# Kernel tuning notes

Hardware: AMD Instinct MI355X
Metric: run time of the kernel (lower is better)

Reference implementation:

```python
import jax, jax.numpy as jnp
import numpy as np

B, N, DIM = 2, 8192, 3
K = 16            # num_neighbours (dilation=1)
R = 2048          # num_representitives
CIN, CL, COUT = 64, 16, 128
K2 = K * K


def _bn(x, g, b):
    # BatchNorm in eval mode with running_mean=0, running_var=1 -> affine
    return x * g + b


def setup_inputs() -> dict:
    key = jax.random.key(0)
    ks = jax.random.split(key, 24)
    r = lambda i, shape, s=1.0: jax.random.normal(ks[i], shape, jnp.float32) * s
    return {
        "points": r(0, (B, N, DIM)),
        "features": r(1, (B, N, CIN)),
        "lift_w": r(2, (CL, DIM), 0.3), "lift_b": r(3, (CL,), 0.1),
        "bn_lift_g": 1.0 + r(4, (CL,), 0.1), "bn_lift_b": r(5, (CL,), 0.1),
        "t1_w": r(6, (K2, DIM * K), 0.1), "t1_b": r(7, (K2,), 0.1),
        "bn1_g": 1.0 + r(8, (K2,), 0.1), "bn1_b": r(9, (K2,), 0.1),
        "t2_w": r(10, (K2, K2), 0.05), "t2_b": r(11, (K2,), 0.1),
        "bn2_g": 1.0 + r(12, (K2,), 0.1), "bn2_b": r(13, (K2,), 0.1),
        "t3_w": r(14, (K2, K2), 0.05), "t3_b": r(15, (K2,), 0.1),
        "bn3_g": 1.0 + r(16, (K2,), 0.1), "bn3_b": r(17, (K2,), 0.1),
        "conv_w": r(18, (COUT, CIN + CL, K), 0.05), "conv_b": r(19, (COUT,), 0.1),
        "rep_idx": jax.random.permutation(ks[20], N)[:R],
    }


def reference(points, features, lift_w, lift_b, bn_lift_g, bn_lift_b,
              t1_w, t1_b, bn1_g, bn1_b, t2_w, t2_b, bn2_g, bn2_b,
              t3_w, t3_b, bn3_g, bn3_b, conv_w, conv_b, rep_idx):
    b, n, _ = points.shape
    # ---- KNN (squared distance is order-equivalent to torch.cdist) ----
    sq = jnp.sum(points * points, -1)                                   # (b,n)
    d2 = sq[:, :, None] + sq[:, None, :] - 2.0 * jnp.einsum('bnd,bmd->bnm', points, points)
    _, idx = jax.lax.top_k(-d2, K + 1)                                  # (b,n,K+1)
    nn_idx = idx[:, :, 1:]                                              # drop self
    # ---- representative sampling + neighbor gather ----
    rep_pos = points[:, rep_idx]                                        # (b,R,3)
    nb_idx = nn_idx[:, rep_idx]                                         # (b,R,K)
    gather = jax.vmap(lambda arr, i: arr[i])
    nbr_pos = gather(points, nb_idx)                                    # (b,R,K,3)
    nbr_feat = gather(features, nb_idx)                                 # (b,R,K,CIN)
    # ---- X_conv ----
    p = (nbr_pos - rep_pos[:, :, None, :]).reshape(b * R, K, DIM)       # centered
    lifted = jax.nn.relu(_bn(p @ lift_w.T + lift_b, bn_lift_g, bn_lift_b))  # (bR,K,CL)
    feat = jnp.concatenate([lifted, nbr_feat.reshape(b * R, K, CIN)], -1)   # (bR,K,CL+CIN)
    pf = p.reshape(b * R, K * DIM)
    h = jax.nn.relu(_bn(pf @ t1_w.T + t1_b, bn1_g, bn1_b))
    h = jax.nn.relu(_bn(h @ t2_w.T + t2_b, bn2_g, bn2_b))
    T = _bn(h @ t3_w.T + t3_b, bn3_g, bn3_b).reshape(b * R, K, K)       # learned transform
    Tf = jnp.einsum('bij,bjc->bic', T, feat)                            # bmm, (bR,K,C)
    # Conv1d(C, COUT, kernel=K) over length K -> single output position
    out = jnp.einsum('bkc,ock->bo', Tf, conv_w) + conv_b                # (bR,COUT)
    return rep_pos, out.reshape(b, R, COUT)
```

## Files before the change

### kernel.cpp

```cpp
#include <hip/hip_runtime.h>
#include <float.h>

#define Bn 2
#define Nn 8192
#define Rr 2048
#define Kk 16
#define CIN 64
#define CL 16
#define COUT 128
#define K2c 256
#define GT (Bn*Rr)
#define FD (CL+CIN)
#define KC (Kk*FD)
#define MG 8

__global__ __launch_bounds__(256) void prep_kernel(
    const float* __restrict__ t1_w, const float* __restrict__ t2_w,
    const float* __restrict__ t3_w, const float* __restrict__ conv_w,
    const float* __restrict__ points,
    float* __restrict__ t1t, float* __restrict__ t2t,
    float* __restrict__ t3t, float* __restrict__ wp,
    float4* __restrict__ pts4)
{
  int i = blockIdx.x * 256 + threadIdx.x;
  if (i < K2c*48) { int j = i / 48, k = i - j*48; t1t[k*K2c + j] = t1_w[i]; }
  if (i < K2c*K2c) { int j = i >> 8, k = i & 255; t2t[k*K2c + j] = t2_w[i]; t3t[k*K2c + j] = t3_w[i]; }
  if (i < COUT*KC) {
    int o = i / KC, ck = i - o*KC;
    int c = ck >> 4, k = ck & 15;
    wp[(k*FD + c)*COUT + o] = conv_w[i];
  }
  if (i < Bn*Nn) {
    float x = points[i*3+0], y = points[i*3+1], z = points[i*3+2];
    float sq = __fadd_rn(__fadd_rn(__fmul_rn(x,x), __fmul_rn(y,y)), __fmul_rn(z,z));
    pts4[i] = make_float4(x, y, z, sq);
  }
}

__global__ __launch_bounds__(512) void knn_kernel(
    const float4* __restrict__ pts4, const int* __restrict__ rep_idx,
    int* __restrict__ nb_idx, float* __restrict__ p_out,
    float* __restrict__ rep_pos_out)
{
  __shared__ float4 ptsS[3072];
  __shared__ unsigned long long coll[8][128];
  int t    = threadIdx.x;
  int lane = t & 63;
  int w    = t >> 6;
  int g    = blockIdx.x * 8 + w;
  int b    = g >> 11;
  int r    = g & 2047;
  int n    = rep_idx[r];
  const float4* pb4 = pts4 + (size_t)b*Nn;
  float4 Q = pb4[n];
  float qx = Q.x, qy = Q.y, qz = Q.z, sqn = Q.w;

  float c0 = FLT_MAX, c1 = FLT_MAX, c2 = FLT_MAX;
  for (int c = 0; c < 3; c++) {
    int base  = c * 3072;
    int count = (c < 2) ? 3072 : 2048;
    __syncthreads();
    for (int i = t; i < count; i += 512) ptsS[i] = pb4[base + i];
    __syncthreads();
    int iters = count >> 6;
    #pragma unroll 4
    for (int j = 0; j < iters; j++) {
      float4 P = ptsS[j*64 + lane];
      float dot = __fmaf_rn(qz, P.z, __fmaf_rn(qy, P.y, __fmul_rn(qx, P.x)));
      float d2  = __fsub_rn(__fadd_rn(sqn, P.w), __fmul_rn(2.0f, dot));
      float nc2 = __builtin_amdgcn_fmed3f(c1, c2, d2);
      float nc1 = __builtin_amdgcn_fmed3f(c0, c1, d2);
      float nc0 = fminf(c0, d2);
      c0 = nc0; c1 = nc1; c2 = nc2;
    }
  }

  float tau = FLT_MAX;
  for (int rnd = 0; rnd < 17; rnd++) {
    float m = c0;
    #pragma unroll
    for (int off = 1; off < 64; off <<= 1) m = fminf(m, __shfl_xor(m, off));
    if (c0 == m) { c0 = c1; c1 = c2; c2 = FLT_MAX; }
    tau = m;
  }

  int cnt = 0;
  for (int c = 0; c < 3; c++) {
    int base  = c * 3072;
    int count = (c < 2) ? 3072 : 2048;
    __syncthreads();
    for (int i = t; i < count; i += 512) ptsS[i] = pb4[base + i];
    __syncthreads();
    int iters = count >> 6;
    #pragma unroll 4
    for (int j = 0; j < iters; j++) {
      float4 P = ptsS[j*64 + lane];
      float dot = __fmaf_rn(qz, P.z, __fmaf_rn(qy, P.y, __fmul_rn(qx, P.x)));
      float d2  = __fsub_rn(__fadd_rn(sqn, P.w), __fmul_rn(2.0f, dot));
      bool pr = (d2 <= tau);
      unsigned long long mask = __ballot(pr);
      if (pr) {
        int pos = cnt + (int)__popcll(mask & ((1ull << lane) - 1ull));
        if (pos < 128) {
          unsigned f = __float_as_uint(d2);
          unsigned mono = f ^ ((unsigned)((int)f >> 31) | 0x80000000u);
          coll[w][pos] = ((unsigned long long)mono << 32) | (unsigned)(base + j*64 + lane);
        }
      }
      cnt += (int)__popcll(mask);
    }
  }
  if (cnt > 128) cnt = 128;

  unsigned long long e1 = (lane < cnt)      ? coll[w][lane]      : ~0ull;
  unsigned long long e2 = (lane + 64 < cnt) ? coll[w][lane + 64] : ~0ull;
  int out_m = 0;
  for (int rnd = 0; rnd < 17; rnd++) {
    unsigned long long myk = (e1 < e2) ? e1 : e2;
    unsigned long long kmin = myk;
    #pragma unroll
    for (int off = 1; off < 64; off <<= 1) {
      unsigned long long o = __shfl_xor(kmin, off);
      kmin = (o < kmin) ? o : kmin;
    }
    if (rnd >= 1 && lane == rnd - 1) out_m = (int)(kmin & 0xFFFFFFFFull);
    if (kmin == e1) e1 = ~0ull;
    else if (kmin == e2) e2 = ~0ull;
  }

  if (lane < 16) {
    nb_idx[g*Kk + lane] = out_m;
    float4 P = pb4[out_m];
    p_out[(g*Kk + lane)*3 + 0] = __fsub_rn(P.x, qx);
    p_out[(g*Kk + lane)*3 + 1] = __fsub_rn(P.y, qy);
    p_out[(g*Kk + lane)*3 + 2] = __fsub_rn(P.z, qz);
  }
  if (lane < 3) rep_pos_out[g*3 + lane] = (lane == 0 ? qx : (lane == 1 ? qy : qz));
}

__device__ __forceinline__ void fma_g(float4& a, float hv, const float4& wv) {
  a.x = fmaf(hv, wv.x, a.x);
  a.y = fmaf(hv, wv.y, a.y);
  a.z = fmaf(hv, wv.z, a.z);
  a.w = fmaf(hv, wv.w, a.w);
}

__global__ __launch_bounds__(256) void mlp_kernel(
    const float* __restrict__ p,
    const float* __restrict__ t1t, const float* __restrict__ t1_b,
    const float* __restrict__ g1v, const float* __restrict__ b1v,
    const float* __restrict__ t2t, const float* __restrict__ t2_b,
    const float* __restrict__ g2v, const float* __restrict__ b2v,
    const float* __restrict__ t3t, const float* __restrict__ t3_b,
    const float* __restrict__ g3v, const float* __restrict__ b3v,
    float* __restrict__ T_out)
{
  __shared__ float pf[48][MG];
  __shared__ float hA[K2c][MG];
  __shared__ float red[4][64][36];
  int t = threadIdx.x;
  int w = t >> 6, l = t & 63;
  int g0 = blockIdx.x * MG;
  for (int e = t; e < MG*48; e += 256) {
    int g = e / 48, k = e - g*48;
    pf[k][g] = p[(size_t)(g0+g)*48 + k];
  }
  __syncthreads();

  float4 acc[8];

#define KLOOP(WSRC, KDIM, HBUF)                                        \
  {                                                                    \
    _Pragma("unroll")                                                  \
    for (int q = 0; q < 8; q++) acc[q] = make_float4(0.f,0.f,0.f,0.f); \
    float4 wb0 = *(const float4*)&WSRC[(size_t)w*K2c + 4*l];           \
    float4 wb1 = (w + 4 < KDIM) ?                                      \
        *(const float4*)&WSRC[(size_t)(w+4)*K2c + 4*l] : wb0;          \
    _Pragma("unroll 2")                                                \
    for (int k = w; k < KDIM; k += 4) {                                \
      float4 wc = wb0; wb0 = wb1;                                      \
      if (k + 8 < KDIM)                                                \
        wb1 = *(const float4*)&WSRC[(size_t)(k+8)*K2c + 4*l];          \
      float4 h0 = *(const float4*)&HBUF[k][0];                         \
      float4 h1 = *(const float4*)&HBUF[k][4];                         \
      fma_g(acc[0], h0.x, wc); fma_g(acc[1], h0.y, wc);                \
      fma_g(acc[2], h0.z, wc); fma_g(acc[3], h0.w, wc);                \
      fma_g(acc[4], h1.x, wc); fma_g(acc[5], h1.y, wc);                \
      fma_g(acc[6], h1.z, wc); fma_g(acc[7], h1.w, wc);                \
    }                                                                  \
  }

#define WRITE_RED()                                                        \
  {                                                                        \
    float4 ra, rb;                                                         \
    ra = make_float4(acc[0].x, acc[1].x, acc[2].x, acc[3].x);              \
    rb = make_float4(acc[4].x, acc[5].x, acc[6].x, acc[7].x);              \
    *(float4*)&red[w][l][0]  = ra; *(float4*)&red[w][l][4]  = rb;          \
    ra = make_float4(acc[0].y, acc[1].y, acc[2].y, acc[3].y);              \
    rb = make_float4(acc[4].y, acc[5].y, acc[6].y, acc[7].y);              \
    *(float4*)&red[w][l][8]  = ra; *(float4*)&red[w][l][12] = rb;          \
    ra = make_float4(acc[0].z, acc[1].z, acc[2].z, acc[3].z);              \
    rb = make_float4(acc[4].z, acc[5].z, acc[6].z, acc[7].z);              \
    *(float4*)&red[w][l][16] = ra; *(float4*)&red[w][l][20] = rb;          \
    ra = make_float4(acc[0].w, acc[1].w, acc[2].w, acc[3].w);              \
    rb = make_float4(acc[4].w, acc[5].w, acc[6].w, acc[7].w);              \
    *(float4*)&red[w][l][24] = ra; *(float4*)&red[w][l][28] = rb;          \
  }

#define REDUCE(SA, SB)                                                     \
  float4 SA = make_float4(0.f,0.f,0.f,0.f), SB = SA;                       \
  {                                                                        \
    int lr = t >> 2, cc = t & 3;                                           \
    _Pragma("unroll")                                                      \
    for (int ww = 0; ww < 4; ww++) {                                       \
      float4 pa = *(const float4*)&red[ww][lr][cc*8 + 0];                  \
      float4 pb = *(const float4*)&red[ww][lr][cc*8 + 4];                  \
      SA.x += pa.x; SA.y += pa.y; SA.z += pa.z; SA.w += pa.w;              \
      SB.x += pb.x; SB.y += pb.y; SB.z += pb.z; SB.w += pb.w;              \
    }                                                                      \
  }

  KLOOP(t1t, 48, pf)
  WRITE_RED()
  __syncthreads();
  {
    REDUCE(sa, sb)
    float bb = t1_b[t], gg = g1v[t], oo = b1v[t];
    float4 va, vb;
    va.x = fmaxf(fmaf(sa.x + bb, gg, oo), 0.f);
    va.y = fmaxf(fmaf(sa.y + bb, gg, oo), 0.f);
    va.z = fmaxf(fmaf(sa.z + bb, gg, oo), 0.f);
    va.w = fmaxf(fmaf(sa.w + bb, gg, oo), 0.f);
    vb.x = fmaxf(fmaf(sb.x + bb, gg, oo), 0.f);
    vb.y = fmaxf(fmaf(sb.y + bb, gg, oo), 0.f);
    vb.z = fmaxf(fmaf(sb.z + bb, gg, oo), 0.f);
    vb.w = fmaxf(fmaf(sb.w + bb, gg, oo), 0.f);
    *(float4*)&hA[t][0] = va;
    *(float4*)&hA[t][4] = vb;
  }
  __syncthreads();

  KLOOP(t2t, K2c, hA)
  __syncthreads();
  WRITE_RED()
  __syncthreads();
  {
    REDUCE(sa, sb)
    float bb = t2_b[t], gg = g2v[t], oo = b2v[t];
    float4 va, vb;
    va.x = fmaxf(fmaf(sa.x + bb, gg, oo), 0.f);
    va.y = fmaxf(fmaf(sa.y + bb, gg, oo), 0.f);
    va.z = fmaxf(fmaf(sa.z + bb, gg, oo), 0.f);
    va.w = fmaxf(fmaf(sa.w + bb, gg, oo), 0.f);
    vb.x = fmaxf(fmaf(sb.x + bb, gg, oo), 0.f);
    vb.y = fmaxf(fmaf(sb.y + bb, gg, oo), 0.f);
    vb.z = fmaxf(fmaf(sb.z + bb, gg, oo), 0.f);
    vb.w = fmaxf(fmaf(sb.w + bb, gg, oo), 0.f);
    *(float4*)&hA[t][0] = va;
    *(float4*)&hA[t][4] = vb;
  }
  __syncthreads();

  KLOOP(t3t, K2c, hA)
  WRITE_RED()
  __syncthreads();
  {
    REDUCE(sa, sb)
    float bb = t3_b[t], gg = g3v[t], oo = b3v[t];
    T_out[(size_t)(g0+0)*K2c + t] = fmaf(sa.x + bb, gg, oo);
    T_out[(size_t)(g0+1)*K2c + t] = fmaf(sa.y + bb, gg, oo);
    T_out[(size_t)(g0+2)*K2c + t] = fmaf(sa.z + bb, gg, oo);
    T_out[(size_t)(g0+3)*K2c + t] = fmaf(sa.w + bb, gg, oo);
    T_out[(size_t)(g0+4)*K2c + t] = fmaf(sb.x + bb, gg, oo);
    T_out[(size_t)(g0+5)*K2c + t] = fmaf(sb.y + bb, gg, oo);
    T_out[(size_t)(g0+6)*K2c + t] = fmaf(sb.z + bb, gg, oo);
    T_out[(size_t)(g0+7)*K2c + t] = fmaf(sb.w + bb, gg, oo);
  }
#undef KLOOP
#undef WRITE_RED
#undef REDUCE
}

__global__ __launch_bounds__(256) void tf_kernel(
    const float* __restrict__ T_in, const float* __restrict__ features,
    const float* __restrict__ p, const int* __restrict__ nb_idx,
    const float* __restrict__ lift_w, const float* __restrict__ lift_b,
    const float* __restrict__ bng, const float* __restrict__ bnb,
    float* __restrict__ Tf)
{
  __shared__ float T_s[8*K2c];
  __shared__ float f_s[8*KC];
  __shared__ float ps[8*48];
  __shared__ int   idxs[128];
  __shared__ float lw[48], lb2[16], lg[16], lo[16];
  int t = threadIdx.x;
  int g0 = blockIdx.x * 8;
  int b = g0 / Rr;
  for (int e = t; e < 8*K2c; e += 256) T_s[e] = T_in[(size_t)g0*K2c + e];
  for (int e = t; e < 8*48;  e += 256) ps[e]  = p[(size_t)g0*48 + e];
  if (t < 128) idxs[t] = nb_idx[g0*16 + t];
  if (t >= 128 && t < 176) lw[t-128]  = lift_w[t-128];
  if (t >= 176 && t < 192) lb2[t-176] = lift_b[t-176];
  if (t >= 192 && t < 208) lg[t-192]  = bng[t-192];
  if (t >= 208 && t < 224) lo[t-208]  = bnb[t-208];
  __syncthreads();

  {
    int wv = t >> 6, ln = t & 63;
    for (int row = wv; row < 128; row += 4) {
      int gg = row >> 4, k = row & 15;
      f_s[gg*KC + k*FD + CL + ln] = features[((size_t)b*Nn + idxs[row])*CIN + ln];
    }
  }
  for (int e = t; e < 2048; e += 256) {
    int gg = e >> 8, rem = e & 255, k = rem >> 4, c = rem & 15;
    float acc = ps[gg*48 + k*3 + 0]*lw[c*3+0] + ps[gg*48 + k*3 + 1]*lw[c*3+1]
              + ps[gg*48 + k*3 + 2]*lw[c*3+2] + lb2[c];
    acc = acc*lg[c] + lo[c];
    f_s[gg*KC + k*FD + c] = fmaxf(acc, 0.f);
  }
  __syncthreads();

  int gg = t >> 5;
  int cl = t & 31;
  for (int ci = cl; ci < FD; ci += 32) {
    float fcol[16];
    #pragma unroll
    for (int j = 0; j < 16; j++) fcol[j] = f_s[gg*KC + j*FD + ci];
    #pragma unroll
    for (int k = 0; k < 16; k++) {
      float acc = 0.f;
      #pragma unroll
      for (int j = 0; j < 16; j++) acc = fmaf(T_s[gg*K2c + k*16 + j], fcol[j], acc);
      Tf[(size_t)(g0+gg)*KC + k*FD + ci] = acc;
    }
  }
}

__global__ __launch_bounds__(256) void gemm_kernel(
    const float* __restrict__ A,
    const float* __restrict__ Bm,
    float* __restrict__ part)
{
  __shared__ float As[16*36];
  __shared__ float Bs[16*COUT];
  int t = threadIdx.x;
  int m0 = blockIdx.x * 32;
  int ky = blockIdx.y;
  int kbase0 = ky * (KC/4);
  float acc[4][4];
  #pragma unroll
  for (int i = 0; i < 4; i++)
    #pragma unroll
    for (int j = 0; j < 4; j++) acc[i][j] = 0.f;
  int tn = t & 31, tm = t >> 5;

  for (int kt = 0; kt < KC/4; kt += 16) {
    int kb = kbase0 + kt;
    {
      int kcol = t & 15, row = t >> 4;
      As[kcol*36 + row]      = A[(size_t)(m0+row)*KC + kb + kcol];
      As[kcol*36 + row + 16] = A[(size_t)(m0+row+16)*KC + kb + kcol];
    }
    {
      int o = t & 127, kk2 = t >> 7;
      #pragma unroll
      for (int p4 = 0; p4 < 8; p4++) {
        int kk = kk2 + p4*2;
        Bs[kk*COUT + o] = Bm[(size_t)(kb+kk)*COUT + o];
      }
    }
    __syncthreads();
    #pragma unroll
    for (int kk = 0; kk < 16; kk++) {
      float4 a4 = *(const float4*)&As[kk*36 + tm*4];
      float4 b4 = *(const float4*)&Bs[kk*COUT + tn*4];
      float av[4] = {a4.x, a4.y, a4.z, a4.w};
      float bv[4] = {b4.x, b4.y, b4.z, b4.w};
      #pragma unroll
      for (int i = 0; i < 4; i++)
        #pragma unroll
        for (int j = 0; j < 4; j++) acc[i][j] = fmaf(av[i], bv[j], acc[i][j]);
    }
    __syncthreads();
  }
  #pragma unroll
  for (int i = 0; i < 4; i++) {
    float4 v = make_float4(acc[i][0], acc[i][1], acc[i][2], acc[i][3]);
    *(float4*)&part[((size_t)ky*GT + m0 + tm*4 + i)*COUT + tn*4] = v;
  }
}

__global__ __launch_bounds__(256) void reduce_kernel(
    const float* __restrict__ part, const float* __restrict__ conv_b,
    float* __restrict__ outp)
{
  int i = blockIdx.x*256 + threadIdx.x;
  const float4* p0 = (const float4*)part;
  const float4* p1 = (const float4*)(part + 1*(size_t)GT*COUT);
  const float4* p2 = (const float4*)(part + 2*(size_t)GT*COUT);
  const float4* p3 = (const float4*)(part + 3*(size_t)GT*COUT);
  float4 a = p0[i], b = p1[i], c = p2[i], d = p3[i];
  float4 e = ((const float4*)conv_b)[i & 31];
  float4 rr;
  rr.x = a.x + b.x + c.x + d.x + e.x;
  rr.y = a.y + b.y + c.y + d.y + e.y;
  rr.z = a.z + b.z + c.z + d.z + e.z;
  rr.w = a.w + b.w + c.w + d.w + e.w;
  ((float4*)outp)[i] = rr;
}

extern "C" void kernel_launch(void* const* d_in, const int* in_sizes, int n_in,
                              void* d_out, int out_size, void* d_ws, size_t ws_size,
                              hipStream_t stream) {
  const float* points   = (const float*)d_in[0];
  const float* features = (const float*)d_in[1];
  const float* lift_w   = (const float*)d_in[2];
  const float* lift_b   = (const float*)d_in[3];
  const float* bn_lift_g= (const float*)d_in[4];
  const float* bn_lift_b= (const float*)d_in[5];
  const float* t1_w     = (const float*)d_in[6];
  const float* t1_b     = (const float*)d_in[7];
  const float* bn1_g    = (const float*)d_in[8];
  const float* bn1_b    = (const float*)d_in[9];
  const float* t2_w     = (const float*)d_in[10];
  const float* t2_b     = (const float*)d_in[11];
  const float* bn2_g    = (const float*)d_in[12];
  const float* bn2_b    = (const float*)d_in[13];
  const float* t3_w     = (const float*)d_in[14];
  const float* t3_b     = (const float*)d_in[15];
  const float* bn3_g    = (const float*)d_in[16];
  const float* bn3_b    = (const float*)d_in[17];
  const float* conv_w   = (const float*)d_in[18];
  const float* conv_b   = (const float*)d_in[19];
  const int*   rep_idx  = (const int*)d_in[20];

  char* ws = (char*)d_ws;
  int*    nb   = (int*)   (ws + 0);
  float*  p    = (float*) (ws + 262144);
  float*  T    = (float*) (ws + 1048576);
  float*  Tf   = (float*) (ws + 5242880);
  float*  wp   = (float*) (ws + 26214400);
  float*  t1t  = (float*) (ws + 26869760);
  float*  t2t  = (float*) (ws + 26918912);
  float*  t3t  = (float*) (ws + 27181056);
  float*  part = (float*) (ws + 33554432);
  float4* pts4 = (float4*)(ws + 41943040);

  float* rep_pos = (float*)d_out;
  float* outp    = (float*)d_out + (size_t)GT*3;

  prep_kernel<<<640, 256, 0, stream>>>(t1_w, t2_w, t3_w, conv_w, points,
                                       t1t, t2t, t3t, wp, pts4);
  knn_kernel<<<GT/8, 512, 0, stream>>>(pts4, rep_idx, nb, p, rep_pos);
  mlp_kernel<<<GT/MG, 256, 0, stream>>>(p, t1t, t1_b, bn1_g, bn1_b,
                                        t2t, t2_b, bn2_g, bn2_b,
                                        t3t, t3_b, bn3_g, bn3_b, T);
  tf_kernel<<<GT/8, 256, 0, stream>>>(T, features, p, nb,
                                      lift_w, lift_b, bn_lift_g, bn_lift_b, Tf);
  dim3 ggrid(GT/32, 4);
  gemm_kernel<<<ggrid, 256, 0, stream>>>(Tf, wp, part);
  reduce_kernel<<<(GT*COUT/4)/256, 256, 0, stream>>>(part, conv_b, outp);
}
```

Before: 226.0 us.

## Fuse Tf bmm, conv GEMM and reduction into one kernel

Merges the T·feat batched matmul, the conv GEMM against the packed weights, and the split-K reduction into a single kernel. Tf stays in registers and shared memory, so it is never written to and read back from global memory, and the partial-sum buffer plus two launches go away. Each block now streams the full 1280x128 weight matrix from global/L2 for only 8 groups, which lowers weight reuse compared with the 32-row GEMM tile. Shared memory use per block grows.

```diff
diff --git a/kernel.cpp b/kernel.cpp
--- a/kernel.cpp
+++ b/kernel.cpp
@@ -281,18 +281,20 @@
 #undef REDUCE
 }
 
-__global__ __launch_bounds__(256) void tf_kernel(
+__global__ __launch_bounds__(256) void tfgemm_kernel(
     const float* __restrict__ T_in, const float* __restrict__ features,
     const float* __restrict__ p, const int* __restrict__ nb_idx,
     const float* __restrict__ lift_w, const float* __restrict__ lift_b,
     const float* __restrict__ bng, const float* __restrict__ bnb,
-    float* __restrict__ Tf)
+    const float* __restrict__ wp, const float* __restrict__ conv_b,
+    float* __restrict__ outp)
 {
+  __shared__ float f_s[8*KC];
   __shared__ float T_s[8*K2c];
-  __shared__ float f_s[8*KC];
   __shared__ float ps[8*48];
   __shared__ int   idxs[128];
   __shared__ float lw[48], lb2[16], lg[16], lo[16];
+  __shared__ float red[4][8][COUT];
   int t = threadIdx.x;
   int g0 = blockIdx.x * 8;
   int b = g0 / Rr;
@@ -323,91 +325,63 @@
 
   int gg = t >> 5;
   int cl = t & 31;
-  for (int ci = cl; ci < FD; ci += 32) {
-    float fcol[16];
-    #pragma unroll
-    for (int j = 0; j < 16; j++) fcol[j] = f_s[gg*KC + j*FD + ci];
-    #pragma unroll
-    for (int k = 0; k < 16; k++) {
-      float acc = 0.f;
+  float tfreg[3][16];
+  {
+    int ii = 0;
+    for (int ci = cl; ci < FD; ci += 32, ii++) {
+      float fcol[16];
       #pragma unroll
-      for (int j = 0; j < 16; j++) acc = fmaf(T_s[gg*K2c + k*16 + j], fcol[j], acc);
-      Tf[(size_t)(g0+gg)*KC + k*FD + ci] = acc;
-    }
-  }
-}
-
-__global__ __launch_bounds__(256) void gemm_kernel(
-    const float* __restrict__ A,
-    const float* __restrict__ Bm,
-    float* __restrict__ part)
-{
-  __shared__ float As[16*36];
-  __shared__ float Bs[16*COUT];
-  int t = threadIdx.x;
-  int m0 = blockIdx.x * 32;
-  int ky = blockIdx.y;
-  int kbase0 = ky * (KC/4);
-  float acc[4][4];
+      for (int j = 0; j < 16; j++) fcol[j] = f_s[gg*KC + j*FD + ci];
+      #pragma unroll
+      for (int k = 0; k < 16; k++) {
+        float acc = 0.f;
+        #pragma unroll
+        for (int j = 0; j < 16; j++) acc = fmaf(T_s[gg*K2c + k*16 + j], fcol[j], acc);
+        tfreg[ii][k] = acc;
+      }
+    }
+  }
+  __syncthreads();
+
+  {
+    int ii = 0;
+    for (int ci = cl; ci < FD; ci += 32, ii++) {
+      #pragma unroll
+      for (int k = 0; k < 16; k++) {
+        f_s[(k*FD + ci)*8 + gg] = tfreg[ii][k];
+      }
+    }
+  }
+  __syncthreads();
+
+  int w = t >> 6, l = t & 63;
+  float2 acc2[8];
   #pragma unroll
-  for (int i = 0; i < 4; i++)
-    #pragma unroll
-    for (int j = 0; j < 4; j++) acc[i][j] = 0.f;
-  int tn = t & 31, tm = t >> 5;
-
-  for (int kt = 0; kt < KC/4; kt += 16) {
-    int kb = kbase0 + kt;
-    {
-      int kcol = t & 15, row = t >> 4;
-      As[kcol*36 + row]      = A[(size_t)(m0+row)*KC + kb + kcol];
-      As[kcol*36 + row + 16] = A[(size_t)(m0+row+16)*KC + kb + kcol];
-    }
-    {
-      int o = t & 127, kk2 = t >> 7;
-      #pragma unroll
-      for (int p4 = 0; p4 < 8; p4++) {
-        int kk = kk2 + p4*2;
-        Bs[kk*COUT + o] = Bm[(size_t)(kb+kk)*COUT + o];
-      }
-    }
-    __syncthreads();
-    #pragma unroll
-    for (int kk = 0; kk < 16; kk++) {
-      float4 a4 = *(const float4*)&As[kk*36 + tm*4];
-      float4 b4 = *(const float4*)&Bs[kk*COUT + tn*4];
-      float av[4] = {a4.x, a4.y, a4.z, a4.w};
-      float bv[4] = {b4.x, b4.y, b4.z, b4.w};
-      #pragma unroll
-      for (int i = 0; i < 4; i++)
-        #pragma unroll
-        for (int j = 0; j < 4; j++) acc[i][j] = fmaf(av[i], bv[j], acc[i][j]);
-    }
-    __syncthreads();
+  for (int q = 0; q < 8; q++) acc2[q] = make_float2(0.f, 0.f);
+  for (int kc = w; kc < KC; kc += 4) {
+    float2 wv = *(const float2*)&wp[(size_t)kc*COUT + 2*l];
+    float4 h0 = *(const float4*)&f_s[kc*8 + 0];
+    float4 h1 = *(const float4*)&f_s[kc*8 + 4];
+    acc2[0].x = fmaf(h0.x, wv.x, acc2[0].x); acc2[0].y = fmaf(h0.x, wv.y, acc2[0].y);
+    acc2[1].x = fmaf(h0.y, wv.x, acc2[1].x); acc2[1].y = fmaf(h0.y, wv.y, acc2[1].y);
+    acc2[2].x = fmaf(h0.z, wv.x, acc2[2].x); acc2[2].y = fmaf(h0.z, wv.y, acc2[2].y);
+    acc2[3].x = fmaf(h0.w, wv.x, acc2[3].x); acc2[3].y = fmaf(h0.w, wv.y, acc2[3].y);
+    acc2[4].x = fmaf(h1.x, wv.x, acc2[4].x); acc2[4].y = fmaf(h1.x, wv.y, acc2[4].y);
+    acc2[5].x = fmaf(h1.y, wv.x, acc2[5].x); acc2[5].y = fmaf(h1.y, wv.y, acc2[5].y);
+    acc2[6].x = fmaf(h1.z, wv.x, acc2[6].x); acc2[6].y = fmaf(h1.z, wv.y, acc2[6].y);
+    acc2[7].x = fmaf(h1.w, wv.x, acc2[7].x); acc2[7].y = fmaf(h1.w, wv.y, acc2[7].y);
   }
   #pragma unroll
-  for (int i = 0; i < 4; i++) {
-    float4 v = make_float4(acc[i][0], acc[i][1], acc[i][2], acc[i][3]);
-    *(float4*)&part[((size_t)ky*GT + m0 + tm*4 + i)*COUT + tn*4] = v;
-  }
-}
-
-__global__ __launch_bounds__(256) void reduce_kernel(
-    const float* __restrict__ part, const float* __restrict__ conv_b,
-    float* __restrict__ outp)
-{
-  int i = blockIdx.x*256 + threadIdx.x;
-  const float4* p0 = (const float4*)part;
-  const float4* p1 = (const float4*)(part + 1*(size_t)GT*COUT);
-  const float4* p2 = (const float4*)(part + 2*(size_t)GT*COUT);
-  const float4* p3 = (const float4*)(part + 3*(size_t)GT*COUT);
-  float4 a = p0[i], b = p1[i], c = p2[i], d = p3[i];
-  float4 e = ((const float4*)conv_b)[i & 31];
-  float4 rr;
-  rr.x = a.x + b.x + c.x + d.x + e.x;
-  rr.y = a.y + b.y + c.y + d.y + e.y;
-  rr.z = a.z + b.z + c.z + d.z + e.z;
-  rr.w = a.w + b.w + c.w + d.w + e.w;
-  ((float4*)outp)[i] = rr;
+  for (int q = 0; q < 8; q++) {
+    *(float2*)&red[w][q][2*l] = acc2[q];
+  }
+  __syncthreads();
+
+  for (int e = t; e < 8*COUT; e += 256) {
+    int q = e >> 7, o = e & 127;
+    float s = red[0][q][o] + red[1][q][o] + red[2][q][o] + red[3][q][o] + conv_b[o];
+    outp[(size_t)(g0+q)*COUT + o] = s;
+  }
 }
 
 extern "C" void kernel_launch(void* const* d_in, const int* in_sizes, int n_in,
@@ -439,12 +413,10 @@
   int*    nb   = (int*)   (ws + 0);
   float*  p    = (float*) (ws + 262144);
   float*  T    = (float*) (ws + 1048576);
-  float*  Tf   = (float*) (ws + 5242880);
   float*  wp   = (float*) (ws + 26214400);
   float*  t1t  = (float*) (ws + 26869760);
   float*  t2t  = (float*) (ws + 26918912);
   float*  t3t  = (float*) (ws + 27181056);
-  float*  part = (float*) (ws + 33554432);
   float4* pts4 = (float4*)(ws + 41943040);
 
   float* rep_pos = (float*)d_out;
@@ -456,9 +428,7 @@
   mlp_kernel<<<GT/MG, 256, 0, stream>>>(p, t1t, t1_b, bn1_g, bn1_b,
                                         t2t, t2_b, bn2_g, bn2_b,
                                         t3t, t3_b, bn3_g, bn3_b, T);
-  tf_kernel<<<GT/8, 256, 0, stream>>>(T, features, p, nb,
-                                      lift_w, lift_b, bn_lift_g, bn_lift_b, Tf);
-  dim3 ggrid(GT/32, 4);
-  gemm_kernel<<<ggrid, 256, 0, stream>>>(Tf, wp, part);
-  reduce_kernel<<<(GT*COUT/4)/256, 256, 0, stream>>>(part, conv_b, outp);
-}
+  tfgemm_kernel<<<GT/8, 256, 0, stream>>>(T, features, p, nb,
+                                          lift_w, lift_b, bn_lift_g, bn_lift_b,
+                                          wp, conv_b, outp);
+}
```

After: 329.4 us. +45.8%, slower.
